# Optimization experiments

Measured on AMD Instinct MI355X. Metric: run time of the kernel, lower is better.

## Reference

```python
import jax, jax.numpy as jnp
import numpy as np

SR = 48000
MAX_DUR = 5.0
N_AUDIO = 480000  # 10 s @ 48 kHz
K_IR = int(SR * MAX_DUR)  # 240000 taps


def setup_inputs() -> dict:
    key = jax.random.key(0)
    k1, k2 = jax.random.split(key)
    audio = jax.random.normal(k1, (N_AUDIO,), dtype=jnp.float32)
    impulse_response = jax.random.normal(k2, (K_IR,), dtype=jnp.float32)
    return {"audio": audio, "impulse_response": impulse_response}


def reference(audio, impulse_response):
    # torch: pad audio with (K-1) zeros, then conv1d (= cross-correlation, no flip)
    K = impulse_response.shape[0]
    a_pad = jnp.concatenate([audio, jnp.zeros((K - 1,), dtype=audio.dtype)])
    # out[t] = sum_k a_pad[t+k] * ir[k], valid correlation -> length N
    out = jnp.correlate(a_pad, impulse_response, mode="valid")
    # trailing peak normalization
    return out / jnp.max(jnp.abs(out))
```

## Files before the change

kernel.cpp:

```cpp
#include <hip/hip_runtime.h>

typedef unsigned int u32;


constexpr int N_AUDIO = 480000;
constexpr int M_FFT   = 1048576;

constexpr size_t OFF_C0   = 0;
constexpr size_t OFF_C1   = (size_t)M_FFT * 8;
constexpr size_t OFF_SLOT = OFF_C1 + (size_t)M_FFT * 8;

#define SW(i) ((i) + ((i) >> 4))
constexpr int LSZ = 1088;

struct F2 { float x, y; };
constexpr double D_PI = 3.14159265358979323846264338327950288;
constexpr double tay_sin(double x) {
    double t = x, s = x, x2 = x * x;
    for (int k = 1; k <= 11; ++k) { t *= -x2 / (double)((2 * k) * (2 * k + 1)); s += t; }
    return s;
}
constexpr double tay_cos(double x) {
    double t = 1.0, s = 1.0, x2 = x * x;
    for (int k = 1; k <= 11; ++k) { t *= -x2 / (double)((2 * k - 1) * (2 * k)); s += t; }
    return s;
}
struct Tab { F2 v[1024]; };
constexpr Tab make_t1() {
    Tab tb{};
    for (int j = 0; j < 1024; ++j) {
        int jj = (j < 512) ? j : j - 1024;
        double a = -2.0 * D_PI * (double)jj / 1024.0;
        tb.v[j] = F2{(float)tay_cos(a), (float)tay_sin(a)};
    }
    return tb;
}
constexpr Tab make_t2() {
    Tab tb{};
    for (int j = 0; j < 1024; ++j) {
        double a = -2.0 * D_PI * (double)j / 1048576.0;
        tb.v[j] = F2{(float)tay_cos(a), (float)tay_sin(a)};
    }
    return tb;
}
__device__ constexpr Tab ROM_T1 = make_t1();
__device__ constexpr Tab ROM_T2 = make_t2();

__device__ __forceinline__ float2 ldrom(const Tab& tb, int i) {
    F2 f = tb.v[i];
    return make_float2(f.x, f.y);
}
__device__ __forceinline__ float2 cmul(float2 a, float2 b) {
    return make_float2(a.x * b.x - a.y * b.y, a.x * b.y + a.y * b.x);
}
__device__ __forceinline__ void stage_tabs(float2* lt1, float2* lt2, int t) {
    #pragma unroll
    for (int q = 0; q < 4; ++q) {
        int i = t + 256 * q;
        lt1[i] = ldrom(ROM_T1, i);
        lt2[i] = ldrom(ROM_T2, i);
    }
}

__device__ __forceinline__ void fft1024_r4(float2 (*A0)[LSZ], float2 (*B0)[LSZ],
                                           const float2* lt1, int t) {
    float2 (*A)[LSZ] = A0;
    float2 (*B)[LSZ] = B0;
    #pragma unroll
    for (int s = 0; s < 5; ++s) {
        const int L  = 1 << (2 * s);
        const int k  = t & (L - 1);
        const int p0 = 4 * t - 3 * k;
        const float2 w  = lt1[k << (9 - 2 * s)];
        const float2 w2 = lt1[k << (8 - 2 * s)];
        #pragma unroll
        for (int j = 0; j < 2; ++j) {
            float2 x0 = A[j][SW(t)];
            float2 x2 = A[j][SW(t + 256)];
            float2 x1 = A[j][SW(t + 512)];
            float2 x3 = A[j][SW(t + 768)];
            float2 wx1 = cmul(w, x1), wx3 = cmul(w, x3);
            float2 u0 = make_float2(x0.x + wx1.x, x0.y + wx1.y);
            float2 u1 = make_float2(x0.x - wx1.x, x0.y - wx1.y);
            float2 u2 = make_float2(x2.x + wx3.x, x2.y + wx3.y);
            float2 u3 = make_float2(x2.x - wx3.x, x2.y - wx3.y);
            float2 a2 = cmul(w2, u2);
            float2 a3 = cmul(w2, u3);
            B[j][SW(p0)]         = make_float2(u0.x + a2.x, u0.y + a2.y);
            B[j][SW(p0 + L)]     = make_float2(u1.x + a3.y, u1.y - a3.x);
            B[j][SW(p0 + 2*L)]   = make_float2(u0.x - a2.x, u0.y - a2.y);
            B[j][SW(p0 + 3*L)]   = make_float2(u1.x - a3.y, u1.y + a3.x);
        }
        __syncthreads();
        float2 (*tmp)[LSZ] = A; A = B; B = tmp;
    }
}

__device__ __forceinline__ void fft512_r4(float2 (*A0)[LSZ], float2 (*B0)[LSZ],
                                          const float2* lt1, int t) {
    float2 (*A)[LSZ] = A0;
    float2 (*B)[LSZ] = B0;
    const int j  = t >> 7;
    const int tt = t & 127;
    #pragma unroll
    for (int s = 0; s < 4; ++s) {
        const int L  = 1 << (2 * s);
        const int k  = tt & (L - 1);
        const int p0 = 4 * tt - 3 * k;
        const float2 w  = lt1[k << (9 - 2 * s)];
        const float2 w2 = lt1[k << (8 - 2 * s)];
        float2 x0 = A[j][SW(tt)];
        float2 x2 = A[j][SW(tt + 128)];
        float2 x1 = A[j][SW(tt + 256)];
        float2 x3 = A[j][SW(tt + 384)];
        float2 wx1 = cmul(w, x1), wx3 = cmul(w, x3);
        float2 u0 = make_float2(x0.x + wx1.x, x0.y + wx1.y);
        float2 u1 = make_float2(x0.x - wx1.x, x0.y - wx1.y);
        float2 u2 = make_float2(x2.x + wx3.x, x2.y + wx3.y);
        float2 u3 = make_float2(x2.x - wx3.x, x2.y - wx3.y);
        float2 a2 = cmul(w2, u2);
        float2 a3 = cmul(w2, u3);
        B[j][SW(p0)]       = make_float2(u0.x + a2.x, u0.y + a2.y);
        B[j][SW(p0 + L)]   = make_float2(u1.x + a3.y, u1.y - a3.x);
        B[j][SW(p0 + 2*L)] = make_float2(u0.x - a2.x, u0.y - a2.y);
        B[j][SW(p0 + 3*L)] = make_float2(u1.x - a3.y, u1.y + a3.x);
        __syncthreads();
        float2 (*tmp)[LSZ] = A; A = B; B = tmp;
    }
    #pragma unroll
    for (int h = 0; h < 2; ++h) {
        int i = tt + 128 * h;
        float2 x0 = A[j][SW(i)];
        float2 x1 = A[j][SW(i + 256)];
        float2 w  = lt1[i << 1];
        float2 wx = cmul(w, x1);
        B[j][SW(i)]       = make_float2(x0.x + wx.x, x0.y + wx.y);
        B[j][SW(i + 256)] = make_float2(x0.x - wx.x, x0.y - wx.y);
    }
    __syncthreads();
}

__global__ __launch_bounds__(256) void kA(const float* __restrict__ a,
                                          const float* __restrict__ b,
                                          float2* __restrict__ outb,
                                          u32* __restrict__ slot) {
    __shared__ float2 buf0[2][LSZ], buf1[2][LSZ], lt1[1024], lt2[1024];
    const int t  = threadIdx.x;
    const int r0 = blockIdx.x * 2;
    if (blockIdx.x == 0 && t == 0) *slot = 0u;
    stage_tabs(lt1, lt2, t);
    #pragma unroll
    for (int q = 0; q < 4; ++q) {
        int c = t + 256 * q;
        int base = c * 1024 + r0;
        float2 av = make_float2(0.f, 0.f), bv = make_float2(0.f, 0.f);
        if (c < 468 || (c == 468 && r0 < 768)) av = *(const float2*)(a + base);
        if (c < 234 || (c == 234 && r0 < 384)) bv = *(const float2*)(b + base);
        buf0[0][SW(c)] = make_float2(av.x, bv.x);
        buf0[1][SW(c)] = make_float2(av.y, bv.y);
    }
    __syncthreads();
    fft1024_r4(buf0, buf1, lt1, t);
    #pragma unroll
    for (int q = 0; q < 4; ++q) {
        int k1 = t + 256 * q;
        #pragma unroll
        for (int j = 0; j < 2; ++j) {
            int e = (r0 + j) * k1;
            float2 w = cmul(lt1[e >> 10], lt2[e & 1023]);
            outb[(r0 + j) * 1024 + k1] = cmul(w, buf1[j][SW(k1)]);
        }
    }
}

__global__ __launch_bounds__(256) void kBC(const float2* __restrict__ in,
                                           float2* __restrict__ gbuf) {
    __shared__ float2 buf0[2][LSZ], buf1[2][LSZ], lt1[1024], lt2[1024];
    const int t = threadIdx.x;
    const int bidx = blockIdx.x;
    const int cA = (bidx == 0) ? 0   : bidx;
    const int cB = (bidx == 0) ? 512 : 1024 - bidx;
    stage_tabs(lt1, lt2, t);
    #pragma unroll
    for (int q = 0; q < 4; ++q) {
        int r = t + 256 * q;
        buf0[0][SW(r)] = in[r * 1024 + cA];
        buf0[1][SW(r)] = in[r * 1024 + cB];
    }
    __syncthreads();
    fft1024_r4(buf0, buf1, lt1, t);
    #pragma unroll
    for (int q = 0; q < 4; ++q) {
        int k2 = t + 256 * q;
        #pragma unroll
        for (int j = 0; j < 2; ++j) {
            float2 z1 = buf1[j][SW(k2)];
            float2 z2;
            if (bidx == 0) z2 = (j == 0) ? buf1[0][SW((1024 - k2) & 1023)]
                                         : buf1[1][SW(1023 - k2)];
            else           z2 = buf1[j ^ 1][SW(1023 - k2)];
            float2 Af  = make_float2(0.5f * (z1.x + z2.x), 0.5f * (z1.y - z2.y));
            float2 cBf = make_float2(0.5f * (z1.y + z2.y), 0.5f * (z1.x - z2.x));
            buf0[j][SW(k2)] = cmul(Af, cBf);
        }
    }
    __syncthreads();
    const float invN2 = 1.0f / 524288.0f;
    #pragma unroll
    for (int j = 0; j < 2; ++j) {
        const int bcol = (j == 0) ? cA : cB;
        const float2 wb = lt2[bcol];
        #pragma unroll
        for (int h = 0; h < 2; ++h) {
            int k2v = t + 256 * h;
            float2 z1 = buf0[j][SW(k2v)];
            int jr, p2;
            if (bidx == 0) { jr = j; p2 = (j == 0) ? (512 - k2v) : (511 - k2v); }
            else           { jr = j ^ 1; p2 = 511 - k2v; }
            float2 z2c = buf0[jr][SW(p2)];
            z2c.y = -z2c.y;
            float2 A2 = make_float2(0.5f * (z1.x + z2c.x), 0.5f * (z1.y + z2c.y));
            float2 D2 = make_float2(0.5f * (z1.x - z2c.x), 0.5f * (z1.y - z2c.y));
            float2 cw = cmul(lt1[k2v], wb);
            float2 iB = cmul(make_float2(cw.y, cw.x), D2);
            float2 Z  = make_float2(A2.x + iB.x, A2.y + iB.y);
            buf1[j][SW(k2v)] = make_float2(Z.x * invN2, -Z.y * invN2);
        }
    }
    __syncthreads();
    fft512_r4(buf1, buf0, lt1, t);
    const int jc = t >> 7, tt = t & 127;
    const int bcol = (jc == 0) ? cA : cB;
    #pragma unroll
    for (int u = 0; u < 4; ++u) {
        int k1 = tt + 128 * u;
        int e2 = 2 * bcol * k1;
        float2 w = cmul(lt1[e2 >> 10], lt2[e2 & 1023]);
        gbuf[bcol * 512 + k1] = cmul(w, buf0[jc][SW(k1)]);
    }
}

__global__ __launch_bounds__(256) void kD(const float2* __restrict__ gbuf,
                                          float2* __restrict__ rawT2,
                                          u32* __restrict__ slot) {
    __shared__ float2 buf0[2][LSZ], buf1[2][LSZ], lt1[1024];
    __shared__ float wmax[4];
    const int t = threadIdx.x;
    const int qb = blockIdx.x;
    #pragma unroll
    for (int q = 0; q < 4; ++q) { int i = t + 256 * q; lt1[i] = ldrom(ROM_T1, i); }
    #pragma unroll
    for (int q = 0; q < 4; ++q) {
        int b = t + 256 * q;
        float4 v = *(const float4*)(gbuf + (size_t)b * 512 + 2 * qb);
        buf0[0][SW(b)] = make_float2(v.x, v.y);
        buf0[1][SW(b)] = make_float2(v.z, v.w);
    }
    __syncthreads();
    fft1024_r4(buf0, buf1, lt1, t);
    float m = 0.0f;
    #pragma unroll
    for (int q = 0; q < 4; ++q) {
        int k2 = t + 256 * q;
        #pragma unroll
        for (int j = 0; j < 2; ++j) {
            int k1 = 2 * qb + j;
            int to = 2 * k1 + 1024 * k2;
            if (to < N_AUDIO) {
                float2 v = buf1[j][SW(k2)];
                rawT2[k1 * 1024 + k2] = make_float2(v.x, -v.y);
                m = fmaxf(m, fmaxf(fabsf(v.x), fabsf(v.y)));
            }
        }
    }
    for (int off = 32; off > 0; off >>= 1) m = fmaxf(m, __shfl_down(m, off, 64));
    if ((t & 63) == 0) wmax[t >> 6] = m;
    __syncthreads();
    if (t == 0) {
        float bm = fmaxf(fmaxf(wmax[0], wmax[1]), fmaxf(wmax[2], wmax[3]));
        atomicMax(slot, __float_as_uint(bm));
    }
}

__global__ __launch_bounds__(256) void kE(const float2* __restrict__ rawT2,
                                          const u32* __restrict__ slot,
                                          float* __restrict__ out) {
    __shared__ float2 tile[64][65];
    const int t  = threadIdx.x;
    const int K0 = (blockIdx.x & 7) * 64;
    const int Q0 = (blockIdx.x >> 3) * 64;
    #pragma unroll
    for (int i = 0; i < 16; ++i) {
        int idx = t + 256 * i;
        int row = idx >> 6, col = idx & 63;
        tile[col][row] = rawT2[(size_t)(K0 + row) * 1024 + Q0 + col];
    }
    __syncthreads();
    const float inv = 1.0f / __uint_as_float(*slot);
    #pragma unroll
    for (int i = 0; i < 16; ++i) {
        int idx = t + 256 * i;
        int cc = idx >> 6, rr = idx & 63;
        int o = (Q0 + cc) * 1024 + 2 * (K0 + rr);
        if (o < N_AUDIO) {
            float2 v = tile[cc][rr];
            *(float2*)(out + o) = make_float2(v.x * inv, v.y * inv);
        }
    }
}

extern "C" void kernel_launch(void* const* d_in, const int* in_sizes, int n_in,
                              void* d_out, int out_size, void* d_ws, size_t ws_size,
                              hipStream_t stream) {
    const float* audio = (const float*)d_in[0];
    const float* ir    = (const float*)d_in[1];
    float* out = (float*)d_out;

    char* ws = (char*)d_ws;
    float2* cb0 = (float2*)(ws + OFF_C0);
    float2* cb1 = (float2*)(ws + OFF_C1);
    u32*    slot = (u32*)(ws + OFF_SLOT);

    kA<<<512, 256, 0, stream>>>(audio, ir, cb1, slot);
    kBC<<<512, 256, 0, stream>>>(cb1, cb0);
    kD<<<256, 256, 0, stream>>>(cb0, cb1, slot);
    kE<<<128, 256, 0, stream>>>((const float2*)cb1, slot, out);
}
```

Measured before the change: 98.90 us.

## Process one FFT column per block in kA/kD and shrink kE tiles

After: 99.03 us. Within noise of the previous version (+0.1%).

```diff
diff --git a/kernel.cpp b/kernel.cpp
--- a/kernel.cpp
+++ b/kernel.cpp
@@ -62,6 +62,7 @@
     }
 }
 
+template<int R>
 __device__ __forceinline__ void fft1024_r4(float2 (*A0)[LSZ], float2 (*B0)[LSZ],
                                            const float2* lt1, int t) {
     float2 (*A)[LSZ] = A0;
@@ -74,7 +75,7 @@
         const float2 w  = lt1[k << (9 - 2 * s)];
         const float2 w2 = lt1[k << (8 - 2 * s)];
         #pragma unroll
-        for (int j = 0; j < 2; ++j) {
+        for (int j = 0; j < R; ++j) {
             float2 x0 = A[j][SW(t)];
             float2 x2 = A[j][SW(t + 256)];
             float2 x1 = A[j][SW(t + 512)];
@@ -144,32 +145,28 @@
                                           const float* __restrict__ b,
                                           float2* __restrict__ outb,
                                           u32* __restrict__ slot) {
-    __shared__ float2 buf0[2][LSZ], buf1[2][LSZ], lt1[1024], lt2[1024];
-    const int t  = threadIdx.x;
-    const int r0 = blockIdx.x * 2;
-    if (blockIdx.x == 0 && t == 0) *slot = 0u;
+    __shared__ float2 buf0[1][LSZ], buf1[1][LSZ], lt1[1024], lt2[1024];
+    const int t = threadIdx.x;
+    const int r = blockIdx.x;
+    if (r == 0 && t == 0) *slot = 0u;
     stage_tabs(lt1, lt2, t);
     #pragma unroll
     for (int q = 0; q < 4; ++q) {
         int c = t + 256 * q;
-        int base = c * 1024 + r0;
-        float2 av = make_float2(0.f, 0.f), bv = make_float2(0.f, 0.f);
-        if (c < 468 || (c == 468 && r0 < 768)) av = *(const float2*)(a + base);
-        if (c < 234 || (c == 234 && r0 < 384)) bv = *(const float2*)(b + base);
-        buf0[0][SW(c)] = make_float2(av.x, bv.x);
-        buf0[1][SW(c)] = make_float2(av.y, bv.y);
-    }
-    __syncthreads();
-    fft1024_r4(buf0, buf1, lt1, t);
+        int base = c * 1024 + r;
+        float av = 0.f, bv = 0.f;
+        if (c < 468 || (c == 468 && r < 768)) av = a[base];
+        if (c < 234 || (c == 234 && r < 384)) bv = b[base];
+        buf0[0][SW(c)] = make_float2(av, bv);
+    }
+    __syncthreads();
+    fft1024_r4<1>(buf0, buf1, lt1, t);
     #pragma unroll
     for (int q = 0; q < 4; ++q) {
         int k1 = t + 256 * q;
-        #pragma unroll
-        for (int j = 0; j < 2; ++j) {
-            int e = (r0 + j) * k1;
-            float2 w = cmul(lt1[e >> 10], lt2[e & 1023]);
-            outb[(r0 + j) * 1024 + k1] = cmul(w, buf1[j][SW(k1)]);
-        }
+        int e = r * k1;
+        float2 w = cmul(lt1[e >> 10], lt2[e & 1023]);
+        outb[r * 1024 + k1] = cmul(w, buf1[0][SW(k1)]);
     }
 }
 
@@ -188,7 +185,7 @@
         buf0[1][SW(r)] = in[r * 1024 + cB];
     }
     __syncthreads();
-    fft1024_r4(buf0, buf1, lt1, t);
+    fft1024_r4<2>(buf0, buf1, lt1, t);
     #pragma unroll
     for (int q = 0; q < 4; ++q) {
         int k2 = t + 256 * q;
@@ -243,34 +240,28 @@
 __global__ __launch_bounds__(256) void kD(const float2* __restrict__ gbuf,
                                           float2* __restrict__ rawT2,
                                           u32* __restrict__ slot) {
-    __shared__ float2 buf0[2][LSZ], buf1[2][LSZ], lt1[1024];
+    __shared__ float2 buf0[1][LSZ], buf1[1][LSZ], lt1[1024];
     __shared__ float wmax[4];
     const int t = threadIdx.x;
-    const int qb = blockIdx.x;
+    const int col = blockIdx.x;
     #pragma unroll
     for (int q = 0; q < 4; ++q) { int i = t + 256 * q; lt1[i] = ldrom(ROM_T1, i); }
     #pragma unroll
     for (int q = 0; q < 4; ++q) {
         int b = t + 256 * q;
-        float4 v = *(const float4*)(gbuf + (size_t)b * 512 + 2 * qb);
-        buf0[0][SW(b)] = make_float2(v.x, v.y);
-        buf0[1][SW(b)] = make_float2(v.z, v.w);
-    }
-    __syncthreads();
-    fft1024_r4(buf0, buf1, lt1, t);
+        buf0[0][SW(b)] = gbuf[(size_t)b * 512 + col];
+    }
+    __syncthreads();
+    fft1024_r4<1>(buf0, buf1, lt1, t);
     float m = 0.0f;
     #pragma unroll
     for (int q = 0; q < 4; ++q) {
         int k2 = t + 256 * q;
-        #pragma unroll
-        for (int j = 0; j < 2; ++j) {
-            int k1 = 2 * qb + j;
-            int to = 2 * k1 + 1024 * k2;
-            if (to < N_AUDIO) {
-                float2 v = buf1[j][SW(k2)];
-                rawT2[k1 * 1024 + k2] = make_float2(v.x, -v.y);
-                m = fmaxf(m, fmaxf(fabsf(v.x), fabsf(v.y)));
-            }
+        int to = 2 * col + 1024 * k2;
+        if (to < N_AUDIO) {
+            float2 v = buf1[0][SW(k2)];
+            rawT2[col * 1024 + k2] = make_float2(v.x, -v.y);
+            m = fmaxf(m, fmaxf(fabsf(v.x), fabsf(v.y)));
         }
     }
     for (int off = 32; off > 0; off >>= 1) m = fmaxf(m, __shfl_down(m, off, 64));
@@ -285,22 +276,22 @@
 __global__ __launch_bounds__(256) void kE(const float2* __restrict__ rawT2,
                                           const u32* __restrict__ slot,
                                           float* __restrict__ out) {
-    __shared__ float2 tile[64][65];
+    __shared__ float2 tile[32][33];
     const int t  = threadIdx.x;
-    const int K0 = (blockIdx.x & 7) * 64;
-    const int Q0 = (blockIdx.x >> 3) * 64;
-    #pragma unroll
-    for (int i = 0; i < 16; ++i) {
+    const int K0 = (blockIdx.x & 15) * 32;
+    const int Q0 = (blockIdx.x >> 4) * 32;
+    #pragma unroll
+    for (int i = 0; i < 4; ++i) {
         int idx = t + 256 * i;
-        int row = idx >> 6, col = idx & 63;
+        int row = idx >> 5, col = idx & 31;
         tile[col][row] = rawT2[(size_t)(K0 + row) * 1024 + Q0 + col];
     }
     __syncthreads();
     const float inv = 1.0f / __uint_as_float(*slot);
     #pragma unroll
-    for (int i = 0; i < 16; ++i) {
+    for (int i = 0; i < 4; ++i) {
         int idx = t + 256 * i;
-        int cc = idx >> 6, rr = idx & 63;
+        int cc = idx >> 5, rr = idx & 31;
         int o = (Q0 + cc) * 1024 + 2 * (K0 + rr);
         if (o < N_AUDIO) {
             float2 v = tile[cc][rr];
@@ -321,8 +312,8 @@
     float2* cb1 = (float2*)(ws + OFF_C1);
     u32*    slot = (u32*)(ws + OFF_SLOT);
 
-    kA<<<512, 256, 0, stream>>>(audio, ir, cb1, slot);
+    kA<<<1024, 256, 0, stream>>>(audio, ir, cb1, slot);
     kBC<<<512, 256, 0, stream>>>(cb1, cb0);
-    kD<<<256, 256, 0, stream>>>(cb0, cb1, slot);
-    kE<<<128, 256, 0, stream>>>((const float2*)cb1, slot, out);
-}
+    kD<<<512, 256, 0, stream>>>(cb0, cb1, slot);
+    kE<<<512, 256, 0, stream>>>((const float2*)cb1, slot, out);
+}
```
